# Optimization experiments

Hardware: AMD Instinct MI355X
Metric: run time of the kernel (lower is better)

The kernel has to match this reference:

```python
import jax, jax.numpy as jnp
import numpy as np
from jax import lax


def _na_indices(size, k):
    # NATTEN-style window: window shifts to stay inside the volume.
    centers = np.arange(size)
    start = np.clip(centers - k // 2, 0, size - k)
    idx = start[:, None] + np.arange(k)[None, :]          # (size, k) neighbor coords
    rel = idx - centers[:, None] + (k - 1)                # (size, k) in [0, 2k-2]
    return jnp.asarray(idx), jnp.asarray(rel)


def _ln(x, g, b):
    mu = jnp.mean(x, axis=-1, keepdims=True)
    var = jnp.mean(jnp.square(x - mu), axis=-1, keepdims=True)
    return (x - mu) * lax.rsqrt(var + 1e-5) * g + b


def setup_inputs() -> dict:
    key = jax.random.key(0)
    ks = jax.random.split(key, 12)
    B, C, H, W, Z = 1, 128, 64, 64, 8
    heads, k = 8, 3
    s = lambda kk, shp: (jax.random.normal(kk, shp, jnp.float32) * 0.02)
    return {
        "x": jax.random.normal(ks[0], (B, C, H, W, Z), jnp.float32),
        "ln1_g": jnp.ones((C,), jnp.float32), "ln1_b": jnp.zeros((C,), jnp.float32),
        "qkv_w": s(ks[1], (C, 3 * C)), "qkv_b": jnp.zeros((3 * C,), jnp.float32),
        "proj_w": s(ks[2], (C, C)), "proj_b": jnp.zeros((C,), jnp.float32),
        "rpb": s(ks[3], (heads, 2 * k - 1, 2 * k - 1, 2 * k - 1)),
        "ln2_g": jnp.ones((C,), jnp.float32), "ln2_b": jnp.zeros((C,), jnp.float32),
        "w1": s(ks[4], (C, 4 * C)), "b1": jnp.zeros((4 * C,), jnp.float32),
        "w2": s(ks[5], (4 * C, C)), "b2": jnp.zeros((C,), jnp.float32),
    }


def reference(x, ln1_g, ln1_b, qkv_w, qkv_b, proj_w, proj_b, rpb,
              ln2_g, ln2_b, w1, b1, w2, b2):
    B, C, H, W, Z = x.shape
    heads = rpb.shape[0]
    k = (rpb.shape[1] + 1) // 2
    hd = C // heads
    K3 = k * k * k

    xp = jnp.transpose(x, (0, 2, 3, 4, 1))                 # (B,H,W,Z,C)
    res1 = xp
    xn = _ln(xp, ln1_g, ln1_b)
    qkv = xn @ qkv_w + qkv_b
    q, kk, v = jnp.split(qkv, 3, axis=-1)

    ih, rh = _na_indices(H, k)
    iw, rw = _na_indices(W, k)
    iz, rz = _na_indices(Z, k)
    Ih = ih[:, None, None, :, None, None]
    Iw = iw[None, :, None, None, :, None]
    Iz = iz[None, None, :, None, None, :]
    # gathered neighborhoods: (B,H,W,Z,k,k,k,C) -> (B,H,W,Z,K3,heads,hd)
    k_n = kk[:, Ih, Iw, Iz, :].reshape(B, H, W, Z, K3, heads, hd)
    v_n = v[:, Ih, Iw, Iz, :].reshape(B, H, W, Z, K3, heads, hd)
    qh = q.reshape(B, H, W, Z, heads, hd) * (hd ** -0.5)

    # scores: (B,H,W,Z,heads,K3)
    scores = jnp.einsum('bxyzne,bxyzmne->bxyznm', qh, k_n)
    bias = rpb[:, rh[:, None, None, :, None, None],
                  rw[None, :, None, None, :, None],
                  rz[None, None, :, None, None, :]]        # (heads,H,W,Z,k,k,k)
    bias = bias.reshape(heads, H, W, Z, K3).transpose(1, 2, 3, 0, 4)
    attn = jax.nn.softmax(scores + bias[None], axis=-1)

    out = jnp.einsum('bxyznm,bxyzmne->bxyzne', attn, v_n).reshape(B, H, W, Z, C)
    out = out @ proj_w + proj_b
    x1 = res1 + out                                        # attention residual
    h = jax.nn.gelu(_ln(x1, ln2_g, ln2_b) @ w1 + b1) @ w2 + b2
    x2 = x1 + h                                            # FFN residual

    enc = jnp.transpose(x2, (0, 4, 1, 2, 3))               # (B,C,H,W,Z)
    skip = enc + x                                         # outer residual
    pooled = lax.reduce_window(skip, -jnp.inf, lax.max,
                               (1, 1, 2, 2, 2), (1, 1, 2, 2, 2), 'VALID')
    return (pooled, skip)
```

## Files before the change

kernel.cpp:

```cpp
#include <hip/hip_runtime.h>
#include <hip/hip_bf16.h>
#include <math.h>

#define NPOS 32768

typedef __hip_bfloat16 bf16;
typedef __attribute__((ext_vector_type(8))) short bf16x8;
typedef __attribute__((ext_vector_type(4))) float f32x4;

__device__ __forceinline__ float bf2f(short s) {
    union { unsigned u; float f; } cv;
    cv.u = ((unsigned)(unsigned short)s) << 16;
    return cv.f;
}

__global__ __launch_bounds__(256) void prep_weights_kernel(
    const float* __restrict__ qkv_w, const float* __restrict__ proj_w,
    const float* __restrict__ w1, const float* __restrict__ w2,
    bf16* __restrict__ wt_qkv, bf16* __restrict__ wt_proj,
    bf16* __restrict__ wt_w1, bf16* __restrict__ wt_w2)
{
    int bi = blockIdx.x;
    const float* src; bf16* dst; int K, M, t;
    if (bi < 48)       { src = qkv_w;  dst = wt_qkv;  K = 128; M = 384; t = bi; }
    else if (bi < 64)  { src = proj_w; dst = wt_proj; K = 128; M = 128; t = bi - 48; }
    else if (bi < 128) { src = w1;     dst = wt_w1;   K = 128; M = 512; t = bi - 64; }
    else               { src = w2;     dst = wt_w2;   K = 512; M = 128; t = bi - 128; }
    int tiles_x = M >> 5;
    int m0 = (t % tiles_x) * 32, k0 = (t / tiles_x) * 32;
    __shared__ float tile[32][33];
    int tx = threadIdx.x & 31, ty = threadIdx.x >> 5;
    #pragma unroll
    for (int i = 0; i < 4; i++)
        tile[ty + i * 8][tx] = src[(size_t)(k0 + ty + i * 8) * M + m0 + tx];
    __syncthreads();
    #pragma unroll
    for (int i = 0; i < 4; i++)
        dst[(size_t)(m0 + ty + i * 8) * K + k0 + tx] = __float2bfloat16(tile[tx][ty + i * 8]);
}

__global__ __launch_bounds__(256) void ln1_transpose_kernel(
    const float* __restrict__ x, const float* __restrict__ g,
    const float* __restrict__ b, bf16* __restrict__ out)
{
    __shared__ float tile[128][65];
    __shared__ float red[2][64][4];
    __shared__ float smu[64], srs[64];
    int n0 = blockIdx.x * 64;
    int tid = threadIdx.x;
    #pragma unroll
    for (int i = 0; i < 32; i++) {
        int idx = i * 256 + tid;
        int c = idx >> 6, nn = idx & 63;
        tile[c][nn] = x[(size_t)c * NPOS + n0 + nn];
    }
    __syncthreads();
    {
        int p = tid >> 2, s = tid & 3;
        float sum = 0.f, ssq = 0.f;
        #pragma unroll
        for (int i = 0; i < 32; i++) {
            float v = tile[s * 32 + i][p];
            sum += v; ssq += v * v;
        }
        red[0][p][s] = sum; red[1][p][s] = ssq;
    }
    __syncthreads();
    if (tid < 64) {
        float s = red[0][tid][0] + red[0][tid][1] + red[0][tid][2] + red[0][tid][3];
        float q = red[1][tid][0] + red[1][tid][1] + red[1][tid][2] + red[1][tid][3];
        float mu = s * (1.f / 128.f);
        float var = q * (1.f / 128.f) - mu * mu;
        smu[tid] = mu;
        srs[tid] = rsqrtf(var + 1e-5f);
    }
    __syncthreads();
    #pragma unroll
    for (int i = 0; i < 32; i++) {
        int idx = i * 256 + tid;
        int nn = idx >> 7, c = idx & 127;
        out[(size_t)(n0 + nn) * 128 + c] =
            __float2bfloat16((tile[c][nn] - smu[nn]) * srs[nn] * g[c] + b[c]);
    }
}

__device__ __forceinline__ float gelu_f(float v) {
    float u = 0.7978845608028654f * (v + 0.044715f * v * v * v);
    return v / (1.f + __expf(-2.f * u));
}

template<int MODE, int BM, int KT>
__global__ __launch_bounds__(256) void gemm_mfma_kernel(
    const bf16* __restrict__ A, const bf16* __restrict__ Bt,
    const float* __restrict__ bias, float* __restrict__ outf, bf16* __restrict__ outb,
    const float* __restrict__ aux0, const float* __restrict__ aux1,
    const float* __restrict__ lng, const float* __restrict__ lnb,
    int N, int M)
{
    constexpr int MF = BM / 32;
    int tid = threadIdx.x;
    int row0 = blockIdx.x * BM;
    int col0 = blockIdx.y * 128;
    int lane = tid & 63, wid = tid >> 6;
    int wr = wid >> 1, wc = wid & 1;
    int lr = lane & 15, kg = lane >> 4;

    const bf16* Ap = A  + (size_t)(row0 + wr * (BM / 2) + lr) * KT + kg * 8;
    const bf16* Bp = Bt + (size_t)(col0 + wc * 64 + lr) * KT + kg * 8;

    f32x4 acc[MF][4] = {};

    #pragma unroll
    for (int k0 = 0; k0 < KT; k0 += 32) {
        bf16x8 af[MF], bf_[4];
        #pragma unroll
        for (int m = 0; m < MF; m++)
            af[m] = *(const bf16x8*)(Ap + (size_t)(m * 16) * KT + k0);
        #pragma unroll
        for (int n = 0; n < 4; n++)
            bf_[n] = *(const bf16x8*)(Bp + (size_t)(n * 16) * KT + k0);
        #pragma unroll
        for (int m = 0; m < MF; m++)
            #pragma unroll
            for (int n = 0; n < 4; n++)
                acc[m][n] = __builtin_amdgcn_mfma_f32_16x16x32_bf16(af[m], bf_[n], acc[m][n], 0, 0, 0);
    }

    if (MODE == 0 || MODE == 2 || MODE == 3) {
        #pragma unroll
        for (int m = 0; m < MF; m++) {
            #pragma unroll
            for (int n = 0; n < 4; n++) {
                int c = col0 + wc * 64 + n * 16 + lr;
                float bv = bias[c];
                #pragma unroll
                for (int j = 0; j < 4; j++) {
                    int r = row0 + wr * (BM / 2) + m * 16 + kg * 4 + j;
                    float v = acc[m][n][j] + bv;
                    if (MODE == 0) {
                        outb[(size_t)r * M + c] = __float2bfloat16(v);
                    } else if (MODE == 2) {
                        outb[(size_t)r * M + c] = __float2bfloat16(gelu_f(v));
                    } else {
                        v += aux1[(size_t)r * 128 + c] + aux0[(size_t)c * N + r];
                        outf[(size_t)c * N + r] = v;
                    }
                }
            }
        }
    } else {
        __shared__ float rsum[64][33];
        __shared__ float rsq[64][33];
        __shared__ float smu[64], srs[64];
        int slot = wc * 16 + lr;
        #pragma unroll
        for (int m = 0; m < MF; m++) {
            #pragma unroll
            for (int j = 0; j < 4; j++) {
                int rloc = wr * (BM / 2) + m * 16 + kg * 4 + j;
                int r = row0 + rloc;
                float ps = 0.f, pq = 0.f;
                #pragma unroll
                for (int n = 0; n < 4; n++) {
                    int c = wc * 64 + n * 16 + lr;
                    float v = acc[m][n][j] + bias[c] + aux0[(size_t)c * N + r];
                    acc[m][n][j] = v;
                    outf[(size_t)r * 128 + c] = v;
                    ps += v; pq += v * v;
                }
                rsum[rloc][slot] = ps;
                rsq[rloc][slot]  = pq;
            }
        }
        __syncthreads();
        if (tid < 64) {
            float s = 0.f, q = 0.f;
            #pragma unroll
            for (int i = 0; i < 32; i++) { s += rsum[tid][i]; q += rsq[tid][i]; }
            float mu = s * (1.f / 128.f);
            float var = q * (1.f / 128.f) - mu * mu;
            smu[tid] = mu;
            srs[tid] = rsqrtf(var + 1e-5f);
        }
        __syncthreads();
        #pragma unroll
        for (int m = 0; m < MF; m++) {
            #pragma unroll
            for (int j = 0; j < 4; j++) {
                int rloc = wr * (BM / 2) + m * 16 + kg * 4 + j;
                int r = row0 + rloc;
                float mu = smu[rloc], rs = srs[rloc];
                #pragma unroll
                for (int n = 0; n < 4; n++) {
                    int c = wc * 64 + n * 16 + lr;
                    float v = (acc[m][n][j] - mu) * rs * lng[c] + lnb[c];
                    outb[(size_t)r * 128 + c] = __float2bfloat16(v);
                }
            }
        }
    }
}

__global__ __launch_bounds__(256) void attn_kernel(
    const bf16* __restrict__ qkv,
    const float* __restrict__ rpb,
    bf16* __restrict__ out)
{
    int t = blockIdx.x * 256 + threadIdx.x;
    int head = t & 7, n = t >> 3;
    int z = n & 7, w = (n >> 3) & 63, h = n >> 9;

    int sh = min(max(h - 1, 0), 61);
    int sw = min(max(w - 1, 0), 61);
    int sz = min(max(z - 1, 0), 5);

    float qf[16];
    {
        const bf16* qp = qkv + (size_t)n * 384 + head * 16;
        bf16x8 q0 = *(const bf16x8*)qp;
        bf16x8 q1 = *(const bf16x8*)(qp + 8);
        #pragma unroll
        for (int e = 0; e < 8; e++) {
            qf[e]     = bf2f(q0[e]) * 0.25f;
            qf[e + 8] = bf2f(q1[e]) * 0.25f;
        }
    }

    const bf16*  kbase = qkv + (size_t)((sh << 9) + (sw << 3) + sz) * 384 + 128 + head * 16;
    const float* rp    = rpb + head * 125 + (sh - h + 2) * 25 + (sw - w + 2) * 5 + (sz - z + 2);

    float sc[27];
    float mx = -1e30f;
    #pragma unroll
    for (int a = 0; a < 3; a++) {
        #pragma unroll
        for (int b = 0; b < 3; b++) {
            #pragma unroll
            for (int c = 0; c < 3; c++) {
                const bf16* kp = kbase + (size_t)(a * 512 + b * 8 + c) * 384;
                bf16x8 k0 = *(const bf16x8*)kp;
                bf16x8 k1 = *(const bf16x8*)(kp + 8);
                float s = 0.f;
                #pragma unroll
                for (int e = 0; e < 8; e++) s = fmaf(qf[e], bf2f(k0[e]), s);
                #pragma unroll
                for (int e = 0; e < 8; e++) s = fmaf(qf[e + 8], bf2f(k1[e]), s);
                s += rp[a * 25 + b * 5 + c];
                sc[a * 9 + b * 3 + c] = s;
                mx = fmaxf(mx, s);
            }
        }
    }

    float sum = 0.f;
    #pragma unroll
    for (int m = 0; m < 27; m++) {
        float e = __expf(sc[m] - mx);
        sc[m] = e;
        sum += e;
    }
    float inv = 1.f / sum;

    float o[16] = {};
    #pragma unroll
    for (int a = 0; a < 3; a++) {
        #pragma unroll
        for (int b = 0; b < 3; b++) {
            #pragma unroll
            for (int c = 0; c < 3; c++) {
                const bf16* vp = kbase + (size_t)(a * 512 + b * 8 + c) * 384 + 128;
                bf16x8 v0 = *(const bf16x8*)vp;
                bf16x8 v1 = *(const bf16x8*)(vp + 8);
                float pm = sc[a * 9 + b * 3 + c];
                #pragma unroll
                for (int e = 0; e < 8; e++) {
                    o[e]     = fmaf(pm, bf2f(v0[e]), o[e]);
                    o[e + 8] = fmaf(pm, bf2f(v1[e]), o[e + 8]);
                }
            }
        }
    }

    short os[16];
    #pragma unroll
    for (int e = 0; e < 16; e++) {
        union { bf16 b; short s; } cv;
        cv.b = __float2bfloat16(o[e] * inv);
        os[e] = cv.s;
    }
    bf16* op = out + (size_t)n * 128 + head * 16;
    *(bf16x8*)op       = *(bf16x8*)os;
    *(bf16x8*)(op + 8) = *(bf16x8*)(os + 8);
}

__global__ __launch_bounds__(256) void pool_kernel(
    const float* __restrict__ skip, float* __restrict__ pooled)
{
    int t = blockIdx.x * 256 + threadIdx.x;
    if (t >= 128 * 32 * 32 * 4) return;
    int oz = t & 3, ow = (t >> 2) & 31, oh = (t >> 7) & 31, c = t >> 12;
    const float* base = skip + (size_t)c * 32768 + (oh * 2) * 512 + (ow * 2) * 8 + oz * 2;
    float m = -INFINITY;
    #pragma unroll
    for (int dh = 0; dh < 2; dh++)
        #pragma unroll
        for (int dw = 0; dw < 2; dw++)
            #pragma unroll
            for (int dz = 0; dz < 2; dz++)
                m = fmaxf(m, base[dh * 512 + dw * 8 + dz]);
    pooled[t] = m;
}

extern "C" void kernel_launch(void* const* d_in, const int* in_sizes, int n_in,
                              void* d_out, int out_size, void* d_ws, size_t ws_size,
                              hipStream_t stream) {
    const float* x      = (const float*)d_in[0];
    const float* ln1_g  = (const float*)d_in[1];
    const float* ln1_b  = (const float*)d_in[2];
    const float* qkv_w  = (const float*)d_in[3];
    const float* qkv_b  = (const float*)d_in[4];
    const float* proj_w = (const float*)d_in[5];
    const float* proj_b = (const float*)d_in[6];
    const float* rpb    = (const float*)d_in[7];
    const float* ln2_g  = (const float*)d_in[8];
    const float* ln2_b  = (const float*)d_in[9];
    const float* w1     = (const float*)d_in[10];
    const float* b1     = (const float*)d_in[11];
    const float* w2     = (const float*)d_in[12];
    const float* b2     = (const float*)d_in[13];

    const int N = NPOS;
    char* wsc = (char*)d_ws;
    bf16*  buf0 = (bf16*)wsc;
    bf16*  buf1 = (bf16*)(wsc + (size_t)N * 128 * 2);
    float* buf2 = (float*)(wsc + (size_t)N * 128 * 2 + (size_t)N * 512 * 2);
    char*  wts  = wsc + (size_t)N * 128 * 2 + (size_t)N * 512 * 2 + (size_t)N * 128 * 4;
    bf16* wt_qkv  = (bf16*)wts;
    bf16* wt_proj = wt_qkv  + 384 * 128;
    bf16* wt_w1   = wt_proj + 128 * 128;
    bf16* wt_w2   = wt_w1   + 512 * 128;

    float* out_pooled = (float*)d_out;
    float* out_skip   = (float*)d_out + 524288;

    prep_weights_kernel<<<192, 256, 0, stream>>>(qkv_w, proj_w, w1, w2,
                                                 wt_qkv, wt_proj, wt_w1, wt_w2);

    ln1_transpose_kernel<<<N / 64, 256, 0, stream>>>(x, ln1_g, ln1_b, buf0);

    gemm_mfma_kernel<0, 128, 128><<<dim3(N / 128, 3), 256, 0, stream>>>(
        buf0, wt_qkv, qkv_b, nullptr, buf1, nullptr, nullptr, nullptr, nullptr, N, 384);

    attn_kernel<<<(N * 8) / 256, 256, 0, stream>>>(buf1, rpb, buf0);

    gemm_mfma_kernel<4, 64, 128><<<dim3(N / 64, 1), 256, 0, stream>>>(
        buf0, wt_proj, proj_b, buf2, buf0, x, nullptr, ln2_g, ln2_b, N, 128);

    gemm_mfma_kernel<2, 128, 128><<<dim3(N / 128, 4), 256, 0, stream>>>(
        buf0, wt_w1, b1, nullptr, buf1, nullptr, nullptr, nullptr, nullptr, N, 512);

    gemm_mfma_kernel<3, 64, 512><<<dim3(N / 64, 1), 256, 0, stream>>>(
        buf1, wt_w2, b2, out_skip, nullptr, x, buf2, nullptr, nullptr, N, 128);

    pool_kernel<<<(524288 + 255) / 256, 256, 0, stream>>>(out_skip, out_pooled);
}
```

Measured before the change: 209.6 us.

## Stage GEMM tiles through LDS with register prefetch and store residual as bf16

Reworks the MFMA GEMM so each block loads coalesced 64-wide K slices of A and B into padded shared memory. The next slice is prefetched into registers while MFMAs run on the current one. This replaces per-lane strided global fragment loads that reloaded each fragment in every wave. Separately, the attention-residual intermediate x1 is stored in bf16 instead of fp32, which halves that buffer's traffic. The cost is added sync barriers and lost precision in the residual path.

```diff
diff --git a/kernel.cpp b/kernel.cpp
--- a/kernel.cpp
+++ b/kernel.cpp
@@ -89,15 +89,22 @@
     return v / (1.f + __expf(-2.f * u));
 }
 
-template<int MODE, int BM, int KT>
+template<int MODE, int KT, int BM>
 __global__ __launch_bounds__(256) void gemm_mfma_kernel(
     const bf16* __restrict__ A, const bf16* __restrict__ Bt,
     const float* __restrict__ bias, float* __restrict__ outf, bf16* __restrict__ outb,
-    const float* __restrict__ aux0, const float* __restrict__ aux1,
+    bf16* __restrict__ outb2,
+    const float* __restrict__ aux0, const bf16* __restrict__ aux1b,
     const float* __restrict__ lng, const float* __restrict__ lnb,
     int N, int M)
 {
     constexpr int MF = BM / 32;
+    constexpr int NSTEP = KT / 64;
+    constexpr int SMEM_BYTES = BM * 144 + 128 * 144;
+    __shared__ __align__(16) char smem[SMEM_BYTES];
+    bf16 (*As)[72] = (bf16(*)[72])smem;
+    bf16 (*Bs)[72] = (bf16(*)[72])(smem + BM * 144);
+
     int tid = threadIdx.x;
     int row0 = blockIdx.x * BM;
     int col0 = blockIdx.y * 128;
@@ -105,25 +112,61 @@
     int wr = wid >> 1, wc = wid & 1;
     int lr = lane & 15, kg = lane >> 4;
 
-    const bf16* Ap = A  + (size_t)(row0 + wr * (BM / 2) + lr) * KT + kg * 8;
-    const bf16* Bp = Bt + (size_t)(col0 + wc * 64 + lr) * KT + kg * 8;
-
     f32x4 acc[MF][4] = {};
-
-    #pragma unroll
-    for (int k0 = 0; k0 < KT; k0 += 32) {
-        bf16x8 af[MF], bf_[4];
-        #pragma unroll
-        for (int m = 0; m < MF; m++)
-            af[m] = *(const bf16x8*)(Ap + (size_t)(m * 16) * KT + k0);
-        #pragma unroll
-        for (int n = 0; n < 4; n++)
-            bf_[n] = *(const bf16x8*)(Bp + (size_t)(n * 16) * KT + k0);
-        #pragma unroll
-        for (int m = 0; m < MF; m++)
+    bf16x8 ra[MF], rb[4];
+
+    #pragma unroll
+    for (int i = 0; i < MF; i++) {
+        int c = tid + i * 256;
+        ra[i] = *(const bf16x8*)(A + (size_t)(row0 + (c >> 3)) * KT + (c & 7) * 8);
+    }
+    #pragma unroll
+    for (int i = 0; i < 4; i++) {
+        int c = tid + i * 256;
+        rb[i] = *(const bf16x8*)(Bt + (size_t)(col0 + (c >> 3)) * KT + (c & 7) * 8);
+    }
+
+    for (int s = 0; s < NSTEP; s++) {
+        if (s > 0) __syncthreads();
+        #pragma unroll
+        for (int i = 0; i < MF; i++) {
+            int c = tid + i * 256;
+            *(bf16x8*)&As[c >> 3][(c & 7) * 8] = ra[i];
+        }
+        #pragma unroll
+        for (int i = 0; i < 4; i++) {
+            int c = tid + i * 256;
+            *(bf16x8*)&Bs[c >> 3][(c & 7) * 8] = rb[i];
+        }
+        __syncthreads();
+        if (s + 1 < NSTEP) {
+            int k0 = (s + 1) * 64;
+            #pragma unroll
+            for (int i = 0; i < MF; i++) {
+                int c = tid + i * 256;
+                ra[i] = *(const bf16x8*)(A + (size_t)(row0 + (c >> 3)) * KT + k0 + (c & 7) * 8);
+            }
+            #pragma unroll
+            for (int i = 0; i < 4; i++) {
+                int c = tid + i * 256;
+                rb[i] = *(const bf16x8*)(Bt + (size_t)(col0 + (c >> 3)) * KT + k0 + (c & 7) * 8);
+            }
+        }
+        #pragma unroll
+        for (int ks = 0; ks < 2; ks++) {
+            bf16x8 af[MF], bf_[4];
+            #pragma unroll
+            for (int m = 0; m < MF; m++)
+                af[m] = *(const bf16x8*)&As[wr * (BM / 2) + m * 16 + lr][ks * 32 + kg * 8];
             #pragma unroll
             for (int n = 0; n < 4; n++)
-                acc[m][n] = __builtin_amdgcn_mfma_f32_16x16x32_bf16(af[m], bf_[n], acc[m][n], 0, 0, 0);
+                bf_[n] = *(const bf16x8*)&Bs[wc * 64 + n * 16 + lr][ks * 32 + kg * 8];
+            #pragma unroll
+            for (int m = 0; m < MF; m++)
+                #pragma unroll
+                for (int n = 0; n < 4; n++)
+                    acc[m][n] = __builtin_amdgcn_mfma_f32_16x16x32_bf16(af[m], bf_[n], acc[m][n], 0, 0, 0);
+        }
     }
 
     if (MODE == 0 || MODE == 2 || MODE == 3) {
@@ -142,16 +185,18 @@
                     } else if (MODE == 2) {
                         outb[(size_t)r * M + c] = __float2bfloat16(gelu_f(v));
                     } else {
-                        v += aux1[(size_t)r * 128 + c] + aux0[(size_t)c * N + r];
+                        v += __bfloat162float(aux1b[(size_t)r * 128 + c]) + aux0[(size_t)c * N + r];
                         outf[(size_t)c * N + r] = v;
                     }
                 }
             }
         }
     } else {
-        __shared__ float rsum[64][33];
-        __shared__ float rsq[64][33];
-        __shared__ float smu[64], srs[64];
+        __syncthreads();
+        float (*rsum)[33] = (float(*)[33])smem;
+        float (*rsq)[33]  = (float(*)[33])(smem + 8448);
+        float* smu = (float*)(smem + 16896);
+        float* srs = (float*)(smem + 17152);
         int slot = wc * 16 + lr;
         #pragma unroll
         for (int m = 0; m < MF; m++) {
@@ -165,7 +210,7 @@
                     int c = wc * 64 + n * 16 + lr;
                     float v = acc[m][n][j] + bias[c] + aux0[(size_t)c * N + r];
                     acc[m][n][j] = v;
-                    outf[(size_t)r * 128 + c] = v;
+                    outb[(size_t)r * 128 + c] = __float2bfloat16(v);
                     ps += v; pq += v * v;
                 }
                 rsum[rloc][slot] = ps;
@@ -194,7 +239,7 @@
                 for (int n = 0; n < 4; n++) {
                     int c = wc * 64 + n * 16 + lr;
                     float v = (acc[m][n][j] - mu) * rs * lng[c] + lnb[c];
-                    outb[(size_t)r * 128 + c] = __float2bfloat16(v);
+                    outb2[(size_t)r * 128 + c] = __float2bfloat16(v);
                 }
             }
         }
@@ -331,10 +376,10 @@
 
     const int N = NPOS;
     char* wsc = (char*)d_ws;
-    bf16*  buf0 = (bf16*)wsc;
-    bf16*  buf1 = (bf16*)(wsc + (size_t)N * 128 * 2);
-    float* buf2 = (float*)(wsc + (size_t)N * 128 * 2 + (size_t)N * 512 * 2);
-    char*  wts  = wsc + (size_t)N * 128 * 2 + (size_t)N * 512 * 2 + (size_t)N * 128 * 4;
+    bf16*  buf0  = (bf16*)wsc;
+    bf16*  buf1  = (bf16*)(wsc + (size_t)N * 128 * 2);
+    bf16*  buf2b = (bf16*)(wsc + (size_t)N * 128 * 2 + (size_t)N * 512 * 2);
+    char*  wts   = wsc + (size_t)N * 128 * 2 + (size_t)N * 512 * 2 + (size_t)N * 128 * 2;
     bf16* wt_qkv  = (bf16*)wts;
     bf16* wt_proj = wt_qkv  + 384 * 128;
     bf16* wt_w1   = wt_proj + 128 * 128;
@@ -349,18 +394,18 @@
     ln1_transpose_kernel<<<N / 64, 256, 0, stream>>>(x, ln1_g, ln1_b, buf0);
 
     gemm_mfma_kernel<0, 128, 128><<<dim3(N / 128, 3), 256, 0, stream>>>(
-        buf0, wt_qkv, qkv_b, nullptr, buf1, nullptr, nullptr, nullptr, nullptr, N, 384);
+        buf0, wt_qkv, qkv_b, nullptr, buf1, nullptr, nullptr, nullptr, nullptr, nullptr, N, 384);
 
     attn_kernel<<<(N * 8) / 256, 256, 0, stream>>>(buf1, rpb, buf0);
 
-    gemm_mfma_kernel<4, 64, 128><<<dim3(N / 64, 1), 256, 0, stream>>>(
-        buf0, wt_proj, proj_b, buf2, buf0, x, nullptr, ln2_g, ln2_b, N, 128);
+    gemm_mfma_kernel<4, 128, 64><<<dim3(N / 64, 1), 256, 0, stream>>>(
+        buf0, wt_proj, proj_b, nullptr, buf2b, buf0, x, nullptr, ln2_g, ln2_b, N, 128);
 
     gemm_mfma_kernel<2, 128, 128><<<dim3(N / 128, 4), 256, 0, stream>>>(
-        buf0, wt_w1, b1, nullptr, buf1, nullptr, nullptr, nullptr, nullptr, N, 512);
-
-    gemm_mfma_kernel<3, 64, 512><<<dim3(N / 64, 1), 256, 0, stream>>>(
-        buf1, wt_w2, b2, out_skip, nullptr, x, buf2, nullptr, nullptr, N, 128);
+        buf0, wt_w1, b1, nullptr, buf1, nullptr, nullptr, nullptr, nullptr, nullptr, N, 512);
+
+    gemm_mfma_kernel<3, 512, 64><<<dim3(N / 64, 1), 256, 0, stream>>>(
+        buf1, wt_w2, b2, out_skip, nullptr, nullptr, x, buf2b, nullptr, nullptr, N, 128);
 
     pool_kernel<<<(524288 + 255) / 256, 256, 0, stream>>>(out_skip, out_pooled);
 }
```

Measured after the change: 176.0 us. 1.19x faster.
